# Kernel optimization log

Measured on AMD Instinct MI355X. Metric: run time of the kernel, lower is better.

The kernel has to match this reference:

```python
import jax, jax.numpy as jnp
import numpy as np

B, C, H, W = 8, 192, 128, 128
NUM_HEADS = 4
EPS = 1e-12  # torch F.normalize default eps


def _conv(x, w, groups=1):
    # NCHW conv, stride 1, SAME padding (kernel 1x1 or 3x3 with pad 1)
    return jax.lax.conv_general_dilated(
        x, w, window_strides=(1, 1), padding='SAME',
        dimension_numbers=('NCHW', 'OIHW', 'NCHW'),
        feature_group_count=groups)


def setup_inputs() -> dict:
    key = jax.random.key(0)
    ks = jax.random.split(key, 7)
    s = 0.02
    x = jax.random.normal(ks[0], (B, C, H, W), dtype=jnp.float32)
    cn = jax.random.normal(ks[1], (B, C, H, W), dtype=jnp.float32)
    cn_conv1_w = jax.random.normal(ks[2], (C, C, 1, 1), dtype=jnp.float32) * s
    cn_conv3_w = jax.random.normal(ks[3], (C, C, 3, 3), dtype=jnp.float32) * s
    qkv_w = jax.random.normal(ks[4], (3 * C, C, 1, 1), dtype=jnp.float32) * s
    qkv_dw_w = jax.random.normal(ks[5], (3 * C, 1, 3, 3), dtype=jnp.float32) * s
    proj_w = jax.random.normal(ks[6], (C, C, 1, 1), dtype=jnp.float32) * s
    temperature = jnp.ones((NUM_HEADS, 1, 1), dtype=jnp.float32)
    return {'x': x, 'cn': cn, 'cn_conv1_w': cn_conv1_w, 'cn_conv3_w': cn_conv3_w,
            'qkv_w': qkv_w, 'qkv_dw_w': qkv_dw_w, 'proj_w': proj_w,
            'temperature': temperature}


def reference(x, cn, cn_conv1_w, cn_conv3_w, qkv_w, qkv_dw_w, proj_w, temperature):
    b, c, h, w = x.shape
    ch = c // NUM_HEADS

    # color-naming feature branch: 1x1 conv then 3x3 conv
    cn_f = _conv(_conv(cn, cn_conv1_w), cn_conv3_w)

    # qkv: 1x1 conv then depthwise 3x3 conv (groups = 3*dim)
    qkv = _conv(_conv(x, qkv_w), qkv_dw_w, groups=3 * c)
    q, k, v = jnp.split(qkv, 3, axis=1)

    def to_heads(t):  # (b, c, h, w) -> (b, head, c/head, h*w)
        return t.reshape(b, NUM_HEADS, ch, h * w)

    def l2n(t):  # L2 normalize over spatial (last) dim, torch-style eps clamp
        return t / jnp.maximum(jnp.linalg.norm(t, axis=-1, keepdims=True), EPS)

    q = l2n(to_heads(q))
    k = l2n(to_heads(k))
    v = to_heads(v)
    cn_h = l2n(to_heads(cn_f))

    # cn_as_value=False, cn_only=False: q = normalize(q + normalized cn)
    q = l2n(q + cn_h)

    # transposed (channel) attention: [b, head, ch, ch]
    attn = jax.nn.softmax(jnp.einsum('bhcs,bhds->bhcd', q, k) * temperature, axis=-1)
    out = jnp.einsum('bhcd,bhds->bhcs', attn, v).reshape(b, c, h, w)
    return _conv(out, proj_w)
```

## Files before the change

kernel.cpp:

```cpp
#include <hip/hip_runtime.h>
#include <hip/hip_bf16.h>

typedef _Float16 f16;
typedef _Float16 f16x8 __attribute__((ext_vector_type(8)));
typedef float f32x4 __attribute__((ext_vector_type(4)));

#define NB 8
#define NC 192
#define NC3 576
#define NS 16384
#define NHD 4

#define OFF_X16   (0ll)
#define OFF_CN16  (50331648ll)
#define OFF_CN1   (100663296ll)
#define OFF_CNF   (150994944ll)
#define OFF_QKVD  (201326592ll)
#define OFF_NORMS (352321536ll)
#define OFF_G1    (352346112ll)
#define OFF_G2    (352641024ll)
#define OFF_ZPAD  (352935936ll)
#define OFF_ATTN  (352936960ll)
#define OFF_W116  (353231872ll)
#define OFF_WQ16  (353305600ll)
#define OFF_W3P   (353526784ll)
#define OFF_MCOMB (354190336ll)
#define OFF_WDWT  (354780160ll)
#define OFF_G1P   (100663296ll)
#define OFF_G2P   (110100480ll)
#define OFF_NPART (119537664ll)

__device__ __forceinline__ void async16(const void* g, void* l) {
  __builtin_amdgcn_global_load_lds(
      (const __attribute__((address_space(1))) unsigned int*)g,
      (__attribute__((address_space(3))) unsigned int*)l, 16, 0, 0);
}
#define MFMA(a,b,c) __builtin_amdgcn_mfma_f32_16x16x32_f16((a),(b),(c),0,0,0)

__global__ void k_wcast(const float* __restrict__ w1, const float* __restrict__ wq,
                        const float* __restrict__ w3, const float* __restrict__ wdw,
                        f16* __restrict__ w1o, f16* __restrict__ wqo,
                        f16* __restrict__ w3p, f16* __restrict__ wdwT)
{
  int idx = blockIdx.x * 256 + threadIdx.x;
  if (idx < 36864) {
    w1o[idx] = (f16)w1[idx];
  } else if (idx < 147456) {
    int i = idx - 36864;
    wqo[i] = (f16)wq[i];
  } else if (idx < 479232) {
    int i = idx - 147456;
    int tap = i / 36864;
    int rem = i % 36864;
    w3p[i] = (f16)w3[(size_t)rem * 9 + tap];
  } else if (idx < 484416) {
    int i = idx - 479232;
    int tap = i / 576;
    int gc = i % 576;
    wdwT[i] = (f16)wdw[(size_t)gc * 9 + tap];
  }
}

__global__ __launch_bounds__(256)
void k_cast_t(const float* __restrict__ xin, const float* __restrict__ cnin,
              f16* __restrict__ xo, f16* __restrict__ cno)
{
  __shared__ f16 tile[64 * 66];
  int b = blockIdx.z & 7;
  const float* in = (blockIdx.z >= 8) ? cnin : xin;
  f16* out = (blockIdx.z >= 8) ? cno : xo;
  int s0 = blockIdx.x * 64, c0 = blockIdx.y * 64;
  int t = threadIdx.x;
  int sl = t & 63, cq = t >> 6;
#pragma unroll
  for (int r = 0; r < 16; ++r) {
    int cl = r * 4 + cq;
    float v = in[((size_t)b * NC + c0 + cl) * NS + s0 + sl];
    tile[cl * 66 + sl] = (f16)v;
  }
  __syncthreads();
  int cl2 = t & 63, sq = t >> 6;
#pragma unroll
  for (int r = 0; r < 16; ++r) {
    int sl2 = r * 4 + sq;
    out[((size_t)b * NS + s0 + sl2) * NC + c0 + cl2] = tile[cl2 * 66 + sl2];
  }
}

__global__ __launch_bounds__(256, 2)
void k_gemm_act(const f16* __restrict__ act, const f16* __restrict__ wt,
                f16* __restrict__ out)
{
  __shared__ f16 At[256 * 32];
  __shared__ f16 Bt[64 * 32];
  const int tid = threadIdx.x;
  const int b = blockIdx.z;
  const int s0 = blockIdx.x * 256;
  const int n0 = blockIdx.y * 64;
  const int w = tid >> 6, lane = tid & 63, quad = lane >> 4, l16 = lane & 15;
  const f16* actB = act + (size_t)b * NS * NC;

  const f32x4 Z = {0.f, 0.f, 0.f, 0.f};
  f32x4 acc[4][4];
#pragma unroll
  for (int i = 0; i < 4; ++i)
#pragma unroll
    for (int j = 0; j < 4; ++j) acc[i][j] = Z;

  for (int kc = 0; kc < 6; ++kc) {
    const int k0 = kc * 32;
#pragma unroll
    for (int i = 0; i < 4; ++i) {
      int r = i * 64 + (w << 4) + (lane >> 2);
      int col = k0 + ((((lane & 3) + (r >> 2)) & 3) << 3);
      async16(actB + (size_t)(s0 + r) * NC + col, At + (size_t)(i * 64 + (w << 4)) * 32);
    }
    {
      int rb = (w << 4) + (lane >> 2);
      int colb = k0 + ((((lane & 3) + (rb >> 2)) & 3) << 3);
      async16(wt + (size_t)(n0 + rb) * NC + colb, Bt + (size_t)(w << 4) * 32);
    }
    __syncthreads();

    f16x8 bf[4];
#pragma unroll
    for (int nt = 0; nt < 4; ++nt) {
      int n = nt * 16 + l16;
      int p = (quad - (n >> 2)) & 3;
      bf[nt] = *(const f16x8*)(Bt + n * 32 + p * 8);
    }
#pragma unroll
    for (int mt = 0; mt < 4; ++mt) {
      int m = w * 64 + mt * 16 + l16;
      int p = (quad - (m >> 2)) & 3;
      f16x8 af = *(const f16x8*)(At + m * 32 + p * 8);
#pragma unroll
      for (int nt = 0; nt < 4; ++nt) acc[mt][nt] = MFMA(af, bf[nt], acc[mt][nt]);
    }
    __syncthreads();
  }
#pragma unroll
  for (int mt = 0; mt < 4; ++mt)
#pragma unroll
    for (int r = 0; r < 4; ++r) {
      int sg = s0 + w * 64 + mt * 16 + quad * 4 + r;
      f16* o = out + ((size_t)b * NS + sg) * NC + n0;
#pragma unroll
      for (int nt = 0; nt < 4; ++nt) o[nt * 16 + l16] = (f16)acc[mt][nt][r];
    }
}

__global__ __launch_bounds__(256, 2)
void k_conv3(const f16* __restrict__ act, const f16* __restrict__ w3p,
             f16* __restrict__ out, const f16* __restrict__ zpad)
{
  __shared__ f16 At[256 * 32];
  __shared__ f16 Bt[64 * 32];
  const int tid = threadIdx.x;
  const int b = blockIdx.z;
  const int s0 = blockIdx.x * 256;
  const int n0 = blockIdx.y * 64;
  const int w = tid >> 6, lane = tid & 63, quad = lane >> 4, l16 = lane & 15;
  const f16* actB = act + (size_t)b * NS * NC;

  const f32x4 Z = {0.f, 0.f, 0.f, 0.f};
  f32x4 acc[4][4];
#pragma unroll
  for (int i = 0; i < 4; ++i)
#pragma unroll
    for (int j = 0; j < 4; ++j) acc[i][j] = Z;

  for (int tap = 0; tap < 9; ++tap) {
    const int dy = tap / 3 - 1, dx = tap % 3 - 1;
    const int off = dy * 128 + dx;
    const f16* wt = w3p + (size_t)tap * NC * NC;
    for (int kc = 0; kc < 6; ++kc) {
      const int k0 = kc * 32;
#pragma unroll
      for (int i = 0; i < 4; ++i) {
        int r = i * 64 + (w << 4) + (lane >> 2);
        int sg = s0 + r;
        int x = sg & 127, y = sg >> 7;
        bool valid = ((unsigned)(x + dx) < 128u) && ((unsigned)(y + dy) < 128u);
        int col = k0 + ((((lane & 3) + (r >> 2)) & 3) << 3);
        const f16* g = valid ? (actB + (size_t)(sg + off) * NC + col) : zpad;
        async16(g, At + (size_t)(i * 64 + (w << 4)) * 32);
      }
      {
        int rb = (w << 4) + (lane >> 2);
        int colb = k0 + ((((lane & 3) + (rb >> 2)) & 3) << 3);
        async16(wt + (size_t)(n0 + rb) * NC + colb, Bt + (size_t)(w << 4) * 32);
      }
      __syncthreads();
      f16x8 bf[4];
#pragma unroll
      for (int nt = 0; nt < 4; ++nt) {
        int n = nt * 16 + l16;
        int p = (quad - (n >> 2)) & 3;
        bf[nt] = *(const f16x8*)(Bt + n * 32 + p * 8);
      }
#pragma unroll
      for (int mt = 0; mt < 4; ++mt) {
        int m = w * 64 + mt * 16 + l16;
        int p = (quad - (m >> 2)) & 3;
        f16x8 af = *(const f16x8*)(At + m * 32 + p * 8);
#pragma unroll
        for (int nt = 0; nt < 4; ++nt) acc[mt][nt] = MFMA(af, bf[nt], acc[mt][nt]);
      }
      __syncthreads();
    }
  }
#pragma unroll
  for (int mt = 0; mt < 4; ++mt)
#pragma unroll
    for (int r = 0; r < 4; ++r) {
      int sg = s0 + w * 64 + mt * 16 + quad * 4 + r;
      f16* o = out + ((size_t)b * NS + sg) * NC + n0;
#pragma unroll
      for (int nt = 0; nt < 4; ++nt) o[nt * 16 + l16] = (f16)acc[mt][nt][r];
    }
}

__global__ __launch_bounds__(256)
void k_dw(const f16* __restrict__ in, const f16* __restrict__ wdwT,
          f16* __restrict__ out, int part)
{
  int idx = blockIdx.x * 256 + threadIdx.x;
  int cg = idx % 24;
  int s = (idx / 24) % NS;
  int b = idx / (24 * NS);
  int x = s & 127, y = s >> 7;
  const f16* ip = in + ((size_t)b * NS + s) * NC + cg * 8;
  const f16* wp = wdwT + part * NC + cg * 8;
  float a[8] = {0.f, 0.f, 0.f, 0.f, 0.f, 0.f, 0.f, 0.f};
#pragma unroll
  for (int t = 0; t < 9; ++t) {
    int dy = t / 3 - 1, dx = t % 3 - 1;
    if (((unsigned)(x + dx) < 128u) && ((unsigned)(y + dy) < 128u)) {
      f16x8 v = *(const f16x8*)(ip + (dy * 128 + dx) * NC);
      f16x8 wv = *(const f16x8*)(wp + t * NC3);
#pragma unroll
      for (int j = 0; j < 8; ++j) a[j] += (float)wv[j] * (float)v[j];
    }
  }
  f16x8 o;
#pragma unroll
  for (int j = 0; j < 8; ++j) o[j] = (f16)a[j];
  *(f16x8*)(out + ((size_t)b * NS + s) * NC3 + part * NC + cg * 8) = o;
}

__global__ __launch_bounds__(64)
void k_e2(const f16* __restrict__ qkvd, const f16* __restrict__ cnf,
          float* __restrict__ G1p, float* __restrict__ G2p,
          float* __restrict__ npart)
{
  __shared__ f16 qT[48 * 72];
  __shared__ f16 kT[48 * 72];
  __shared__ f16 cT[48 * 72];
  int blk = blockIdx.x;
  int split = blk & 31;
  int h = (blk >> 5) & 3;
  int b = blk >> 7;
  int lane = threadIdx.x, quad = lane >> 4, l16 = lane & 15;
  const f32x4 Z = {0.f, 0.f, 0.f, 0.f};
  f32x4 g1[3][3], g2[3][3];
#pragma unroll
  for (int i = 0; i < 3; ++i)
#pragma unroll
    for (int j = 0; j < 3; ++j) { g1[i][j] = Z; g2[i][j] = Z; }
  float q2[3] = {0.f, 0.f, 0.f}, k2[3] = {0.f, 0.f, 0.f};
  float cn2[3] = {0.f, 0.f, 0.f}, qc[3] = {0.f, 0.f, 0.f};

  int sBase = split * 512;
  for (int chunk = 0; chunk < 8; ++chunk) {
    int sb = sBase + chunk * 64;
    const f16* qrow = qkvd + ((size_t)b * NS + sb + lane) * NC3 + h * 48;
    const f16* crow = cnf + ((size_t)b * NS + sb + lane) * NC + h * 48;
    f16x8 qv[6], kv[6], nv[6];
#pragma unroll
    for (int i = 0; i < 6; ++i) {
      qv[i] = *(const f16x8*)(qrow + i * 8);
      kv[i] = *(const f16x8*)(qrow + 192 + i * 8);
      nv[i] = *(const f16x8*)(crow + i * 8);
    }
    __syncthreads();
#pragma unroll
    for (int i = 0; i < 6; ++i)
#pragma unroll
      for (int j = 0; j < 8; ++j) {
        int c = i * 8 + j;
        qT[c * 72 + lane] = qv[i][j];
        kT[c * 72 + lane] = kv[i][j];
        cT[c * 72 + lane] = nv[i][j];
      }
    __syncthreads();
#pragma unroll
    for (int kk = 0; kk < 2; ++kk) {
      int ko = kk * 32 + quad * 8;
      f16x8 bfr[3];
#pragma unroll
      for (int dt = 0; dt < 3; ++dt) {
        bfr[dt] = *(const f16x8*)(kT + (dt * 16 + l16) * 72 + ko);
#pragma unroll
        for (int j = 0; j < 8; ++j) { float kf = (float)bfr[dt][j]; k2[dt] += kf * kf; }
      }
#pragma unroll
      for (int ct = 0; ct < 3; ++ct) {
        f16x8 aq = *(const f16x8*)(qT + (ct * 16 + l16) * 72 + ko);
        f16x8 an = *(const f16x8*)(cT + (ct * 16 + l16) * 72 + ko);
#pragma unroll
        for (int j = 0; j < 8; ++j) {
          float qf = (float)aq[j], nf = (float)an[j];
          q2[ct] += qf * qf; cn2[ct] += nf * nf; qc[ct] += qf * nf;
        }
#pragma unroll
        for (int dt = 0; dt < 3; ++dt) {
          g1[ct][dt] = MFMA(aq, bfr[dt], g1[ct][dt]);
          g2[ct][dt] = MFMA(an, bfr[dt], g2[ct][dt]);
        }
      }
    }
  }
  size_t gbase = ((size_t)((b * NHD + h) * 32 + split)) * 2304;
#pragma unroll
  for (int ct = 0; ct < 3; ++ct)
#pragma unroll
    for (int dt = 0; dt < 3; ++dt)
#pragma unroll
      for (int r = 0; r < 4; ++r) {
        int c = ct * 16 + quad * 4 + r;
        int d = dt * 16 + l16;
        G1p[gbase + c * 48 + d] = g1[ct][dt][r];
        G2p[gbase + c * 48 + d] = g2[ct][dt][r];
      }
#pragma unroll
  for (int t = 0; t < 3; ++t) {
    q2[t] += __shfl_xor(q2[t], 16, 64);  q2[t] += __shfl_xor(q2[t], 32, 64);
    k2[t] += __shfl_xor(k2[t], 16, 64);  k2[t] += __shfl_xor(k2[t], 32, 64);
    cn2[t] += __shfl_xor(cn2[t], 16, 64); cn2[t] += __shfl_xor(cn2[t], 32, 64);
    qc[t] += __shfl_xor(qc[t], 16, 64);  qc[t] += __shfl_xor(qc[t], 32, 64);
  }
  if (lane < 16) {
#pragma unroll
    for (int ct = 0; ct < 3; ++ct) {
      int c = h * 48 + ct * 16 + lane;
      float* np = npart + (((size_t)(b * 32 + split)) * NC + c) * 4;
      np[0] = q2[ct]; np[1] = k2[ct]; np[2] = cn2[ct]; np[3] = qc[ct];
    }
  }
}

__global__ void k_e1b(const float* __restrict__ npart, float* __restrict__ norms)
{
  int idx = blockIdx.x * 256 + threadIdx.x;
  int b = idx / 768;
  int cs = idx % 768;
  const float* p = npart + (size_t)b * 32 * 768 + cs;
  float s = 0.f;
#pragma unroll
  for (int sp = 0; sp < 32; ++sp) s += p[sp * 768];
  norms[idx] = s;
}

__global__ void k_e2b(const float* __restrict__ G1p, const float* __restrict__ G2p,
                      float* __restrict__ G1, float* __restrict__ G2)
{
  int idx = blockIdx.x * 256 + threadIdx.x;
  int bh = idx / 2304;
  int cd = idx % 2304;
  const float* p1 = G1p + ((size_t)bh * 32) * 2304 + cd;
  const float* p2 = G2p + ((size_t)bh * 32) * 2304 + cd;
  float s1 = 0.f, s2 = 0.f;
#pragma unroll
  for (int sp = 0; sp < 32; ++sp) { s1 += p1[sp * 2304]; s2 += p2[sp * 2304]; }
  G1[idx] = s1;
  G2[idx] = s2;
}

__global__ __launch_bounds__(64)
void k_f1(const float* __restrict__ G1, const float* __restrict__ G2,
          const float* __restrict__ norms, const float* __restrict__ temp,
          float* __restrict__ attn)
{
  __shared__ float S[48 * 48];
  int h = blockIdx.x & 3, b = blockIdx.x >> 2;
  int t = threadIdx.x;
  float T = temp[h];
  const float EPS = 1e-12f;
#pragma unroll
  for (int i = 0; i < 36; ++i) {
    int idx = i * 64 + t;
    int c = idx / 48, d = idx % 48;
    const float* np = norms + ((size_t)b * NC + h * 48 + c) * 4;
    float q2 = np[0], cn2 = np[2], qc = np[3];
    float nq = fmaxf(sqrtf(q2), EPS);
    float ncn = fmaxf(sqrtf(cn2), EPS);
    float k2 = norms[((size_t)b * NC + h * 48 + d) * 4 + 1];
    float nk = fmaxf(sqrtf(k2), EPS);
    float ss = q2 / (nq * nq) + 2.f * qc / (nq * ncn) + cn2 / (ncn * ncn);
    float nsum = fmaxf(sqrtf(fmaxf(ss, 0.f)), EPS);
    size_t go = (((size_t)(b * NHD + h) * 48 + c) * 48 + d);
    S[idx] = (G1[go] / nq + G2[go] / ncn) / (nsum * nk) * T;
  }
  __syncthreads();
  if (t < 48) {
    float mx = -1e30f;
    for (int d = 0; d < 48; ++d) mx = fmaxf(mx, S[t * 48 + d]);
    float sum = 0.f;
    for (int d = 0; d < 48; ++d) { float e = expf(S[t * 48 + d] - mx); S[t * 48 + d] = e; sum += e; }
    float inv = 1.f / sum;
    float* ap = attn + (((size_t)(b * NHD + h) * 48 + t) * 48);
    for (int d = 0; d < 48; ++d) ap[d] = S[t * 48 + d] * inv;
  }
}

__global__ void k_f2(const float* __restrict__ attn, const float* __restrict__ projw,
                     f16* __restrict__ mcomb)
{
  int idx = blockIdx.x * 256 + threadIdx.x;
  int dg = idx % NC;
  int co = (idx / NC) % NC;
  int b = idx / (NC * NC);
  int h = dg / 48, dl = dg % 48;
  const float* pw = projw + (size_t)co * NC + h * 48;
  const float* at = attn + ((size_t)(b * NHD + h) * 48) * 48 + dl;
  float a = 0.f;
#pragma unroll
  for (int cl = 0; cl < 48; ++cl) a += pw[cl] * at[cl * 48];
  mcomb[idx] = (f16)a;
}

__global__ __launch_bounds__(256, 2)
void k_gemm_out(const f16* __restrict__ mcomb, const f16* __restrict__ qkvd,
                float* __restrict__ out)
{
  __shared__ f16 At[64 * 32];
  __shared__ f16 Bt[256 * 32];
  const int tid = threadIdx.x;
  const int b = blockIdx.z;
  const int s0 = blockIdx.x * 256;
  const int m0 = blockIdx.y * 64;
  const int w = tid >> 6, lane = tid & 63, quad = lane >> 4, l16 = lane & 15;
  const f16* mcB = mcomb + (size_t)b * NC * NC;
  const f16* vB = qkvd + (size_t)b * NS * NC3 + 384;

  const f32x4 Z = {0.f, 0.f, 0.f, 0.f};
  f32x4 acc[4][4];
#pragma unroll
  for (int i = 0; i < 4; ++i)
#pragma unroll
    for (int j = 0; j < 4; ++j) acc[i][j] = Z;

  for (int kc = 0; kc < 6; ++kc) {
    const int k0 = kc * 32;
    {
      int rb = (w << 4) + (lane >> 2);
      int colb = k0 + ((((lane & 3) + (rb >> 2)) & 3) << 3);
      async16(mcB + (size_t)(m0 + rb) * NC + colb, At + (size_t)(w << 4) * 32);
    }
#pragma unroll
    for (int i = 0; i < 4; ++i) {
      int r = i * 64 + (w << 4) + (lane >> 2);
      int col = k0 + ((((lane & 3) + (r >> 2)) & 3) << 3);
      async16(vB + (size_t)(s0 + r) * NC3 + col, Bt + (size_t)(i * 64 + (w << 4)) * 32);
    }
    __syncthreads();
    f16x8 af[4];
#pragma unroll
    for (int mt = 0; mt < 4; ++mt) {
      int m = mt * 16 + l16;
      int p = (quad - (m >> 2)) & 3;
      af[mt] = *(const f16x8*)(At + m * 32 + p * 8);
    }
#pragma unroll
    for (int nt = 0; nt < 4; ++nt) {
      int n = w * 64 + nt * 16 + l16;
      int p = (quad - (n >> 2)) & 3;
      f16x8 bf = *(const f16x8*)(Bt + n * 32 + p * 8);
#pragma unroll
      for (int mt = 0; mt < 4; ++mt) acc[mt][nt] = MFMA(af[mt], bf, acc[mt][nt]);
    }
    __syncthreads();
  }
#pragma unroll
  for (int mt = 0; mt < 4; ++mt)
#pragma unroll
    for (int r = 0; r < 4; ++r) {
      int cog = m0 + mt * 16 + quad * 4 + r;
      float* o = out + ((size_t)b * NC + cog) * NS + s0 + w * 64;
#pragma unroll
      for (int nt = 0; nt < 4; ++nt) o[nt * 16 + l16] = acc[mt][nt][r];
    }
}

extern "C" void kernel_launch(void* const* d_in, const int* in_sizes, int n_in,
                              void* d_out, int out_size, void* d_ws, size_t ws_size,
                              hipStream_t stream) {
  const float* x   = (const float*)d_in[0];
  const float* cn  = (const float*)d_in[1];
  const float* w1  = (const float*)d_in[2];
  const float* w3  = (const float*)d_in[3];
  const float* wq  = (const float*)d_in[4];
  const float* wdw = (const float*)d_in[5];
  const float* wpj = (const float*)d_in[6];
  const float* tmp = (const float*)d_in[7];
  float* out = (float*)d_out;
  char* ws = (char*)d_ws;

  f16* x16    = (f16*)(ws + OFF_X16);
  f16* cn16   = (f16*)(ws + OFF_CN16);
  f16* qkv1p  = (f16*)(ws + OFF_CN16);
  f16* cn1    = (f16*)(ws + OFF_CN1);
  f16* cnf    = (f16*)(ws + OFF_CNF);
  f16* qkvd   = (f16*)(ws + OFF_QKVD);
  float* norms = (float*)(ws + OFF_NORMS);
  float* G1    = (float*)(ws + OFF_G1);
  float* G2    = (float*)(ws + OFF_G2);
  f16* zpad   = (f16*)(ws + OFF_ZPAD);
  float* attn  = (float*)(ws + OFF_ATTN);
  f16* w116   = (f16*)(ws + OFF_W116);
  f16* wq16   = (f16*)(ws + OFF_WQ16);
  f16* w3p    = (f16*)(ws + OFF_W3P);
  f16* mcomb  = (f16*)(ws + OFF_MCOMB);
  f16* wdwT   = (f16*)(ws + OFF_WDWT);
  float* G1p   = (float*)(ws + OFF_G1P);
  float* G2p   = (float*)(ws + OFF_G2P);
  float* npart = (float*)(ws + OFF_NPART);

  hipMemsetAsync(ws + OFF_ZPAD, 0, 1024, stream);

  k_wcast<<<1893, 256, 0, stream>>>(w1, wq, w3, wdw, w116, wq16, w3p, wdwT);
  k_cast_t<<<dim3(256, 3, 16), 256, 0, stream>>>(x, cn, x16, cn16);
  k_gemm_act<<<dim3(64, 3, 8), 256, 0, stream>>>(cn16, w116, cn1);
  k_conv3<<<dim3(64, 3, 8), 256, 0, stream>>>(cn1, w3p, cnf, zpad);
  for (int p = 0; p < 3; ++p) {
    k_gemm_act<<<dim3(64, 3, 8), 256, 0, stream>>>(x16, wq16 + p * 36864, qkv1p);
    k_dw<<<12288, 256, 0, stream>>>(qkv1p, wdwT, qkvd, p);
  }
  k_e2<<<1024, 64, 0, stream>>>(qkvd, cnf, G1p, G2p, npart);
  k_e1b<<<24, 256, 0, stream>>>(npart, norms);
  k_e2b<<<1152, 256, 0, stream>>>(G1p, G2p, G1, G2);
  k_f1<<<32, 64, 0, stream>>>(G1, G2, norms, tmp, attn);
  k_f2<<<1152, 256, 0, stream>>>(attn, wpj, mcomb);
  k_gemm_out<<<dim3(64, 3, 8), 256, 0, stream>>>(mcomb, qkvd, out);

  (void)in_sizes; (void)n_in; (void)out_size; (void)ws_size;
}
```

Baseline: 749.0 us.

## Reuse a haloed activation tile across all nine conv3 taps

The 3x3 conv kernel now loads a 4-row by 130-column activation tile (two output rows plus halo) into shared memory once per K chunk. It reuses that tile for all nine taps instead of reloading a shifted 256-row tile for each tap. Weights for five taps and then four taps are staged together, which cuts the number of barriers. The 1D grid is also remapped so consecutive blocks spread across batch elements. Shared memory grows to about 53 KB, which may limit occupancy under the 2-blocks-per-SM launch bound.

```diff
diff --git a/kernel.cpp b/kernel.cpp
--- a/kernel.cpp
+++ b/kernel.cpp
@@ -154,15 +154,26 @@
 void k_conv3(const f16* __restrict__ act, const f16* __restrict__ w3p,
              f16* __restrict__ out, const f16* __restrict__ zpad)
 {
-  __shared__ f16 At[256 * 32];
-  __shared__ f16 Bt[64 * 32];
+  __shared__ f16 At[4 * 130 * 32];
+  __shared__ f16 Bt[5 * 64 * 32];
   const int tid = threadIdx.x;
-  const int b = blockIdx.z;
-  const int s0 = blockIdx.x * 256;
-  const int n0 = blockIdx.y * 64;
+  const int bid = blockIdx.x;
+  const int swz = (bid & 7) * 192 + (bid >> 3);
+  const int b = swz / 192;
+  const int rem = swz % 192;
+  const int stile = rem / 3;
+  const int nblk = rem % 3;
+  const int y0 = stile * 2;
+  const int s0 = stile * 256;
+  const int n0 = nblk * 64;
   const int w = tid >> 6, lane = tid & 63, quad = lane >> 4, l16 = lane & 15;
   const f16* actB = act + (size_t)b * NS * NC;
 
+  {
+    int pos = tid >> 5, ch = tid & 31;
+    At[((pos >> 1) * 130 + ((pos & 1) ? 129 : 0)) * 32 + ch] = (f16)0.f;
+  }
+
   const f32x4 Z = {0.f, 0.f, 0.f, 0.f};
   f32x4 acc[4][4];
 #pragma unroll
@@ -170,51 +181,86 @@
 #pragma unroll
     for (int j = 0; j < 4; ++j) acc[i][j] = Z;
 
-  for (int tap = 0; tap < 9; ++tap) {
-    const int dy = tap / 3 - 1, dx = tap % 3 - 1;
-    const int off = dy * 128 + dx;
-    const f16* wt = w3p + (size_t)tap * NC * NC;
-    for (int kc = 0; kc < 6; ++kc) {
-      const int k0 = kc * 32;
-#pragma unroll
-      for (int i = 0; i < 4; ++i) {
-        int r = i * 64 + (w << 4) + (lane >> 2);
-        int sg = s0 + r;
-        int x = sg & 127, y = sg >> 7;
-        bool valid = ((unsigned)(x + dx) < 128u) && ((unsigned)(y + dy) < 128u);
-        int col = k0 + ((((lane & 3) + (r >> 2)) & 3) << 3);
-        const f16* g = valid ? (actB + (size_t)(sg + off) * NC + col) : zpad;
-        async16(g, At + (size_t)(i * 64 + (w << 4)) * 32);
-      }
-      {
-        int rb = (w << 4) + (lane >> 2);
-        int colb = k0 + ((((lane & 3) + (rb >> 2)) & 3) << 3);
-        async16(wt + (size_t)(n0 + rb) * NC + colb, Bt + (size_t)(w << 4) * 32);
-      }
-      __syncthreads();
+  const int yrow = y0 - 1 + w;
+  const bool rowok = ((unsigned)yrow < 128u);
+  const f16* arow = actB + (size_t)(yrow * 128) * NC;
+
+  for (int kc = 0; kc < 6; ++kc) {
+    const int k0 = kc * 32;
+#pragma unroll
+    for (int i = 0; i < 8; ++i) {
+      int x = i * 16 + (lane >> 2);
+      int rs = w * 130 + 1 + x;
+      int gsrc = ((lane & 3) + (rs >> 2)) & 3;
+      const f16* g = rowok ? (arow + (size_t)x * NC + k0 + gsrc * 8)
+                           : (const f16*)zpad;
+      async16(g, At + (w * 130 + 1) * 32 + i * 512);
+    }
+#pragma unroll
+    for (int tp = 0; tp < 5; ++tp) {
+      int co = (w << 4) + (lane >> 2);
+      int gsrc = ((lane & 3) + (co >> 2)) & 3;
+      async16(w3p + (size_t)tp * NC * NC + (size_t)(n0 + co) * NC + k0 + gsrc * 8,
+              Bt + (tp * 64 + (w << 4)) * 32);
+    }
+    __syncthreads();
+#pragma unroll
+    for (int tp = 0; tp < 5; ++tp) {
+      const int dy = tp / 3 - 1, dx = tp % 3 - 1;
       f16x8 bf[4];
 #pragma unroll
       for (int nt = 0; nt < 4; ++nt) {
         int n = nt * 16 + l16;
         int p = (quad - (n >> 2)) & 3;
-        bf[nt] = *(const f16x8*)(Bt + n * 32 + p * 8);
+        bf[nt] = *(const f16x8*)(Bt + (tp * 64 + n) * 32 + p * 8);
       }
 #pragma unroll
       for (int mt = 0; mt < 4; ++mt) {
-        int m = w * 64 + mt * 16 + l16;
-        int p = (quad - (m >> 2)) & 3;
-        f16x8 af = *(const f16x8*)(At + m * 32 + p * 8);
+        int m = (w << 6) + mt * 16 + l16;
+        int rr = ((m >> 7) + 1 + dy) * 130 + (m & 127) + 1 + dx;
+        int p = (quad - (rr >> 2)) & 3;
+        f16x8 af = *(const f16x8*)(At + rr * 32 + p * 8);
 #pragma unroll
         for (int nt = 0; nt < 4; ++nt) acc[mt][nt] = MFMA(af, bf[nt], acc[mt][nt]);
       }
-      __syncthreads();
-    }
+    }
+    __syncthreads();
+#pragma unroll
+    for (int tp = 0; tp < 4; ++tp) {
+      int co = (w << 4) + (lane >> 2);
+      int gsrc = ((lane & 3) + (co >> 2)) & 3;
+      async16(w3p + (size_t)(tp + 5) * NC * NC + (size_t)(n0 + co) * NC + k0 + gsrc * 8,
+              Bt + (tp * 64 + (w << 4)) * 32);
+    }
+    __syncthreads();
+#pragma unroll
+    for (int tp = 0; tp < 4; ++tp) {
+      const int tap = tp + 5;
+      const int dy = tap / 3 - 1, dx = tap % 3 - 1;
+      f16x8 bf[4];
+#pragma unroll
+      for (int nt = 0; nt < 4; ++nt) {
+        int n = nt * 16 + l16;
+        int p = (quad - (n >> 2)) & 3;
+        bf[nt] = *(const f16x8*)(Bt + (tp * 64 + n) * 32 + p * 8);
+      }
+#pragma unroll
+      for (int mt = 0; mt < 4; ++mt) {
+        int m = (w << 6) + mt * 16 + l16;
+        int rr = ((m >> 7) + 1 + dy) * 130 + (m & 127) + 1 + dx;
+        int p = (quad - (rr >> 2)) & 3;
+        f16x8 af = *(const f16x8*)(At + rr * 32 + p * 8);
+#pragma unroll
+        for (int nt = 0; nt < 4; ++nt) acc[mt][nt] = MFMA(af, bf[nt], acc[mt][nt]);
+      }
+    }
+    __syncthreads();
   }
 #pragma unroll
   for (int mt = 0; mt < 4; ++mt)
 #pragma unroll
     for (int r = 0; r < 4; ++r) {
-      int sg = s0 + w * 64 + mt * 16 + quad * 4 + r;
+      int sg = s0 + (w << 6) + mt * 16 + quad * 4 + r;
       f16* o = out + ((size_t)b * NS + sg) * NC + n0;
 #pragma unroll
       for (int nt = 0; nt < 4; ++nt) o[nt * 16 + l16] = (f16)acc[mt][nt][r];
@@ -532,7 +578,7 @@
   k_wcast<<<1893, 256, 0, stream>>>(w1, wq, w3, wdw, w116, wq16, w3p, wdwT);
   k_cast_t<<<dim3(256, 3, 16), 256, 0, stream>>>(x, cn, x16, cn16);
   k_gemm_act<<<dim3(64, 3, 8), 256, 0, stream>>>(cn16, w116, cn1);
-  k_conv3<<<dim3(64, 3, 8), 256, 0, stream>>>(cn1, w3p, cnf, zpad);
+  k_conv3<<<1536, 256, 0, stream>>>(cn1, w3p, cnf, zpad);
   for (int p = 0; p < 3; ++p) {
     k_gemm_act<<<dim3(64, 3, 8), 256, 0, stream>>>(x16, wq16 + p * 36864, qkv1p);
     k_dw<<<12288, 256, 0, stream>>>(qkv1p, wdwT, qkvd, p);
```

Result: faster. 705.5 us (-5.8%).
